# Kernel optimization log

Measured on AMD Instinct MI355X. Metric: run time of the kernel, lower is better.

The kernel has to match this reference:

```python
import jax, jax.numpy as jnp
import numpy as np
import math

B, S, E = 2, 2048, 2048
H, NOPE, ROPE, V, KVR, DOWN = 16, 64, 32, 64, 256, 2
QKD = NOPE + ROPE
SCALE = QKD ** -0.5
LOW = 4


def setup_inputs() -> dict:
    key = jax.random.key(0)
    ks = jax.random.split(key, 8)
    def w(k, shape):
        return jax.random.normal(k, shape, jnp.float32) * 0.02
    return {
        "hidden_states": jax.random.normal(ks[0], (B, S, E), jnp.float32),
        "wq": w(ks[1], (H * QKD, E)),
        "wkv_a": w(ks[2], (KVR + ROPE, E)),
        "kv_ln_g": jnp.ones((KVR,), jnp.float32),
        "kv_ln_b": jnp.zeros((KVR,), jnp.float32),
        "wkv_b": w(ks[3], (H * (NOPE + V), KVR)),
        "wo": w(ks[4], (E, H * V)),
        "fc_c_w": w(ks[5], (KVR // LOW, KVR)),
        "fc_c_b": jnp.zeros((KVR // LOW,), jnp.float32),
        "fc_p_w": w(ks[6], (KVR // LOW, KVR)),
        "fc_p_b": jnp.zeros((KVR // LOW,), jnp.float32),
    }


def _layernorm(x, g, b, eps=1e-5):
    m = jnp.mean(x, -1, keepdims=True)
    v = jnp.var(x, -1, keepdims=True)
    return (x - m) * jax.lax.rsqrt(v + eps) * g + b


def _pos_enc(T, d):
    # sinusoidal PE: even dims sin, odd dims cos (interleaved)
    pos = jnp.arange(T, dtype=jnp.float32)[:, None]
    div = jnp.exp(jnp.arange(0, d, 2, dtype=jnp.float32) * (-math.log(10000.0) / d))
    ang = pos * div[None, :]
    return jnp.stack([jnp.sin(ang), jnp.cos(ang)], -1).reshape(T, d)


def _rope(x, cos, sin):
    # complex multiply on adjacent pairs, matching torch.view_as_complex path
    xr = x.reshape(x.shape[:-1] + (-1, 2))
    x0, x1 = xr[..., 0], xr[..., 1]
    return jnp.stack([x0 * cos - x1 * sin, x0 * sin + x1 * cos], -1).reshape(x.shape)


def reference(hidden_states, wq, wkv_a, kv_ln_g, kv_ln_b, wkv_b, wo,
              fc_c_w, fc_c_b, fc_p_w, fc_p_b):
    # q projection -> split nope / rope parts
    q = (hidden_states @ wq.T).reshape(B, S, H, QKD)
    q_nope, q_pe = q[..., :NOPE], q[..., NOPE:]
    # low-rank kv projection -> latent + shared rope key
    kv = hidden_states @ wkv_a.T
    kv_c, k_pe = kv[..., :KVR], kv[..., KVR:]
    kv_c = _layernorm(kv_c, kv_ln_g, kv_ln_b)
    # inline partial RoPE (position_ids = arange)
    pos = jnp.arange(S, dtype=jnp.float32)
    freqs = 1.0 / (10000.0 ** (jnp.arange(0, ROPE, 2, dtype=jnp.float32) / ROPE))
    ang = pos[:, None] * freqs[None, :]  # (S, ROPE//2)
    cos, sin = jnp.cos(ang), jnp.sin(ang)
    q_pe = _rope(q_pe, cos[None, :, None, :], sin[None, :, None, :])
    k_pe = _rope(k_pe, cos[None, :, :], sin[None, :, :])
    # hypernetwork gate (train path): C from downsampled PE, repeat_interleave
    t = -(-S // DOWN)
    P = _pos_enc(S, KVR)
    C = jnp.repeat(_pos_enc(t, KVR), DOWN, axis=0)[:S]
    C2 = C @ fc_c_w.T + fc_c_b
    P2 = P @ fc_p_w.T + fc_p_b
    Wg = jax.nn.sigmoid(C2 @ P2.T)  # (S, S)
    r = jnp.arange(S)
    chunk = ((r[:, None] // DOWN) == (r[None, :] // DOWN)) & \
            ((r[:, None] % DOWN) >= (r[None, :] % DOWN))
    Wg = Wg * chunk.astype(Wg.dtype)
    # temporally merged latent KV (simulated compressed cache)
    kv_t = jnp.einsum('ts,bsc->btc', Wg, kv_c)
    k_pe_t = jnp.einsum('ts,bsr->btr', Wg, k_pe)
    # absorbed wkv_b: q_nope into latent space
    wkv_b3 = wkv_b.reshape(H, NOPE + V, KVR)
    q_abs = jnp.einsum('bshd,hdc->bshc', q_nope, wkv_b3[:, :NOPE])
    scores = (jnp.einsum('bshc,btc->bsht', q_abs, kv_t)
              + jnp.einsum('bshr,btr->bsht', q_pe, k_pe_t)) * SCALE
    # stride-aware causal mask: chunk-boundary keys + diagonal
    visible = ((r[None, :] <= r[:, None]) & (((r[None, :] + 1) % DOWN) == 0)) | \
              (r[None, :] == r[:, None])
    mask = jnp.where(visible, 0.0, -1e9).astype(scores.dtype)
    attn = jax.nn.softmax(scores + mask[:, None, :], axis=-1)
    x = jnp.einsum('bsht,btc->bshc', attn, kv_t)
    out = jnp.einsum('bshc,hdc->bshd', x, wkv_b3[:, NOPE:]).reshape(B, S, H * V)
    return out @ wo.T
```

## Files before the change

kernel.cpp:

```cpp
#include <hip/hip_runtime.h>
#include <hip/hip_bf16.h>
#include <math.h>
#include <stdint.h>

#define B_ 2
#define S_ 2048
#define E_ 2048
#define H_ 16
#define NOPE_ 64
#define ROPE_ 32
#define V_ 64
#define KVR_ 256
#define QKD_ 96
#define SCALE_ 0.10206207261596577f

typedef __hip_bfloat16 bf16;
typedef __attribute__((ext_vector_type(8))) short short8;
typedef __attribute__((ext_vector_type(4))) short short4v;
typedef __attribute__((ext_vector_type(4))) float floatx4;

__device__ __forceinline__ float bf2f(bf16 v) { return __bfloat162float(v); }
__device__ __forceinline__ float s2f(short v) {
    bf16 h = *reinterpret_cast<bf16*>(&v);
    return __bfloat162float(h);
}
__device__ __forceinline__ short f2bf_s(float f) {
    bf16 h = __float2bfloat16(f);
    return *reinterpret_cast<short*>(&h);
}
__device__ __forceinline__ void store_c(float* C, size_t i, float v) { C[i] = v; }
__device__ __forceinline__ void store_c(bf16* C, size_t i, float v) { C[i] = __float2bfloat16(v); }

__device__ __forceinline__ void g2l16(const bf16* g, bf16* l) {
    __builtin_amdgcn_global_load_lds(
        (const __attribute__((address_space(1))) void*)g,
        (__attribute__((address_space(3))) void*)l,
        16, 0, 0);
}

#define CV_N0 1048576
#define CV_N1 (CV_N0 + 393216)
#define CV_N2 (CV_N1 + 262144)
#define CV_N3 (CV_N2 + 65536)
#define CV_N4 (CV_N3 + 98304)
__global__ __launch_bounds__(256) void conv_fused_kernel(const float* __restrict__ hs,
                                                         const float* __restrict__ wq,
                                                         const float* __restrict__ wo,
                                                         const float* __restrict__ wkv_b,
                                                         const float* __restrict__ wkv_a,
                                                         bf16* __restrict__ hs_bf,
                                                         bf16* __restrict__ wq_bf,
                                                         bf16* __restrict__ wo_bf,
                                                         bf16* __restrict__ wkvb_bf,
                                                         bf16* __restrict__ wkva_pad) {
    int i = blockIdx.x * 256 + threadIdx.x;
    const float* src;
    bf16* dst;
    int j;
    if (i < CV_N0)      { src = hs;    dst = hs_bf;   j = i; }
    else if (i < CV_N1) { src = wq;    dst = wq_bf;   j = i - CV_N0; }
    else if (i < CV_N2) { src = wo;    dst = wo_bf;   j = i - CV_N1; }
    else if (i < CV_N3) { src = wkv_b; dst = wkvb_bf; j = i - CV_N2; }
    else if (i < CV_N4) {
        j = i - CV_N3;
        int row = j >> 8;
        short8 r;
        if (row < 288) {
            float4 a = ((const float4*)wkv_a)[2 * j];
            float4 b = ((const float4*)wkv_a)[2 * j + 1];
            r[0] = f2bf_s(a.x); r[1] = f2bf_s(a.y); r[2] = f2bf_s(a.z); r[3] = f2bf_s(a.w);
            r[4] = f2bf_s(b.x); r[5] = f2bf_s(b.y); r[6] = f2bf_s(b.z); r[7] = f2bf_s(b.w);
        } else {
            for (int k = 0; k < 8; ++k) r[k] = 0;
        }
        ((short8*)wkva_pad)[j] = r;
        return;
    } else return;
    float4 a = ((const float4*)src)[2 * j];
    float4 b = ((const float4*)src)[2 * j + 1];
    short8 r;
    r[0] = f2bf_s(a.x); r[1] = f2bf_s(a.y); r[2] = f2bf_s(a.z); r[3] = f2bf_s(a.w);
    r[4] = f2bf_s(b.x); r[5] = f2bf_s(b.y); r[6] = f2bf_s(b.z); r[7] = f2bf_s(b.w);
    ((short8*)dst)[j] = r;
}

__global__ __launch_bounds__(256) void transpose_wkvbT_kernel(const float* __restrict__ wkv_b,
                                                              bf16* __restrict__ wkvbT) {
    int h = blockIdx.x >> 3;
    int d0 = (blockIdx.x & 7) * 8;
    int c = threadIdx.x;
    short8 v;
#pragma unroll
    for (int j = 0; j < 8; ++j) v[j] = f2bf_s(wkv_b[(size_t)(h * 128 + d0 + j) * 256 + c]);
    *(short8*)(void*)&wkvbT[((size_t)h * 256 + c) * 64 + d0] = v;
}

template <typename TC>
__global__ __launch_bounds__(256, 3) void gemm_bt_lds(const bf16* __restrict__ A,
                                                      const bf16* __restrict__ Bm,
                                                      TC* __restrict__ C,
                                                      int M, int N, int K) {
    __shared__ bf16 Asf[128 * 32];
    __shared__ bf16 Bsf[128 * 32];
    int tid = threadIdx.x;
    int lane = tid & 63, w = tid >> 6;
    int q4 = lane >> 4, c16 = lane & 15;
    int wr = w >> 1, wc = w & 1;
    int m0 = blockIdx.y * 128, n0 = blockIdx.x * 128;
    floatx4 acc[4][4];
#pragma unroll
    for (int mi = 0; mi < 4; ++mi)
#pragma unroll
        for (int ni = 0; ni < 4; ++ni) acc[mi][ni] = (floatx4){0.f, 0.f, 0.f, 0.f};

    for (int k0 = 0; k0 < K; k0 += 32) {
        __syncthreads();
#pragma unroll
        for (int i = 0; i < 2; ++i) {
            int c = (w << 6) + lane + i * 256;
            int row = c >> 2, kc = c & 3;
            g2l16(&A[(size_t)(m0 + row) * K + k0 + kc * 8], &Asf[c * 8]);
            g2l16(&Bm[(size_t)(n0 + row) * K + k0 + kc * 8], &Bsf[c * 8]);
        }
        __syncthreads();
        short8 af[4], bfr[4];
#pragma unroll
        for (int mi = 0; mi < 4; ++mi)
            af[mi] = *(const short8*)(const void*)&Asf[(wr * 64 + mi * 16 + c16) * 32 + q4 * 8];
#pragma unroll
        for (int ni = 0; ni < 4; ++ni)
            bfr[ni] = *(const short8*)(const void*)&Bsf[(wc * 64 + ni * 16 + c16) * 32 + q4 * 8];
#pragma unroll
        for (int mi = 0; mi < 4; ++mi)
#pragma unroll
            for (int ni = 0; ni < 4; ++ni)
                acc[mi][ni] = __builtin_amdgcn_mfma_f32_16x16x32_bf16(af[mi], bfr[ni], acc[mi][ni], 0, 0, 0);
    }
#pragma unroll
    for (int mi = 0; mi < 4; ++mi)
#pragma unroll
        for (int ni = 0; ni < 4; ++ni)
#pragma unroll
            for (int r = 0; r < 4; ++r) {
                int row = m0 + wr * 64 + mi * 16 + q4 * 4 + r;
                int col = n0 + wc * 64 + ni * 16 + c16;
                store_c(C, (size_t)row * N + col, acc[mi][ni][r]);
            }
}

__global__ __launch_bounds__(256, 3) void gemm_qkv_fused(const bf16* __restrict__ A,
                                                         const bf16* __restrict__ Bq,
                                                         const bf16* __restrict__ Bkv,
                                                         bf16* __restrict__ Cq,
                                                         float* __restrict__ Ckv,
                                                         int K) {
    __shared__ bf16 Asf[128 * 32];
    __shared__ bf16 Bsf[128 * 32];
    int tid = threadIdx.x;
    int lane = tid & 63, w = tid >> 6;
    int q4 = lane >> 4, c16 = lane & 15;
    int wr = w >> 1, wc = w & 1;
    int bx = blockIdx.x;
    bool isq = bx < 12;
    const bf16* Bm = isq ? Bq : Bkv;
    int n0 = isq ? bx * 128 : (bx - 12) * 128;
    int m0 = blockIdx.y * 128;
    floatx4 acc[4][4];
#pragma unroll
    for (int mi = 0; mi < 4; ++mi)
#pragma unroll
        for (int ni = 0; ni < 4; ++ni) acc[mi][ni] = (floatx4){0.f, 0.f, 0.f, 0.f};

    for (int k0 = 0; k0 < K; k0 += 32) {
        __syncthreads();
#pragma unroll
        for (int i = 0; i < 2; ++i) {
            int c = (w << 6) + lane + i * 256;
            int row = c >> 2, kc = c & 3;
            g2l16(&A[(size_t)(m0 + row) * K + k0 + kc * 8], &Asf[c * 8]);
            g2l16(&Bm[(size_t)(n0 + row) * K + k0 + kc * 8], &Bsf[c * 8]);
        }
        __syncthreads();
        short8 af[4], bfr[4];
#pragma unroll
        for (int mi = 0; mi < 4; ++mi)
            af[mi] = *(const short8*)(const void*)&Asf[(wr * 64 + mi * 16 + c16) * 32 + q4 * 8];
#pragma unroll
        for (int ni = 0; ni < 4; ++ni)
            bfr[ni] = *(const short8*)(const void*)&Bsf[(wc * 64 + ni * 16 + c16) * 32 + q4 * 8];
#pragma unroll
        for (int mi = 0; mi < 4; ++mi)
#pragma unroll
            for (int ni = 0; ni < 4; ++ni)
                acc[mi][ni] = __builtin_amdgcn_mfma_f32_16x16x32_bf16(af[mi], bfr[ni], acc[mi][ni], 0, 0, 0);
    }
#pragma unroll
    for (int mi = 0; mi < 4; ++mi)
#pragma unroll
        for (int ni = 0; ni < 4; ++ni)
#pragma unroll
            for (int r = 0; r < 4; ++r) {
                int row = m0 + wr * 64 + mi * 16 + q4 * 4 + r;
                int col = n0 + wc * 64 + ni * 16 + c16;
                if (isq)
                    Cq[(size_t)row * 1536 + col] = __float2bfloat16(acc[mi][ni][r]);
                else
                    Ckv[(size_t)row * 384 + col] = acc[mi][ni][r];
            }
}

template <typename TC>
__global__ __launch_bounds__(256, 4) void gemm64_lds(const bf16* __restrict__ A, int lda, int aoffz,
                                                     const bf16* __restrict__ Bm, int ldb, int boffz,
                                                     TC* __restrict__ C, int ldc, int coffz,
                                                     int K, float scale) {
    int z = blockIdx.z;
    A += (size_t)z * aoffz;
    Bm += (size_t)z * boffz;
    C += (size_t)z * coffz;
    __shared__ bf16 Asf[64 * 32];
    __shared__ bf16 Bsf[64 * 32];
    int tid = threadIdx.x;
    int lane = tid & 63, w = tid >> 6;
    int q4 = lane >> 4, c16 = lane & 15;
    int m0 = blockIdx.y * 64, n0 = blockIdx.x * 64;
    floatx4 acc[4];
#pragma unroll
    for (int ni = 0; ni < 4; ++ni) acc[ni] = (floatx4){0.f, 0.f, 0.f, 0.f};
    int row = tid >> 2, kc = tid & 3;
    for (int k0 = 0; k0 < K; k0 += 32) {
        __syncthreads();
        g2l16(&A[(size_t)(m0 + row) * lda + k0 + kc * 8], &Asf[tid * 8]);
        g2l16(&Bm[(size_t)(n0 + row) * ldb + k0 + kc * 8], &Bsf[tid * 8]);
        __syncthreads();
        short8 af = *(const short8*)(const void*)&Asf[(w * 16 + c16) * 32 + q4 * 8];
#pragma unroll
        for (int ni = 0; ni < 4; ++ni) {
            short8 bfr = *(const short8*)(const void*)&Bsf[(ni * 16 + c16) * 32 + q4 * 8];
            acc[ni] = __builtin_amdgcn_mfma_f32_16x16x32_bf16(af, bfr, acc[ni], 0, 0, 0);
        }
    }
#pragma unroll
    for (int ni = 0; ni < 4; ++ni)
#pragma unroll
        for (int rr = 0; rr < 4; ++rr)
            store_c(C, (size_t)(m0 + w * 16 + q4 * 4 + rr) * ldc + n0 + ni * 16 + c16,
                    acc[ni][rr] * scale);
}

__global__ __launch_bounds__(256) void ln_rope_kernel(const float* __restrict__ kvraw,
                                                      const float* __restrict__ g,
                                                      const float* __restrict__ bta,
                                                      float* __restrict__ kv_c,
                                                      float* __restrict__ kpe) {
    int r = blockIdx.x;
    int tid = threadIdx.x;
    int lane = tid & 63, w = tid >> 6;
    float x = kvraw[(size_t)r * 384 + tid];
    float v1 = x, v2 = x * x;
#pragma unroll
    for (int o = 32; o; o >>= 1) { v1 += __shfl_down(v1, o); v2 += __shfl_down(v2, o); }
    __shared__ float s1[4], s2[4], stats[2];
    if (lane == 0) { s1[w] = v1; s2[w] = v2; }
    __syncthreads();
    if (tid == 0) {
        float S1 = s1[0] + s1[1] + s1[2] + s1[3];
        float S2 = s2[0] + s2[1] + s2[2] + s2[3];
        float mean = S1 / 256.0f;
        float var = S2 / 256.0f - mean * mean;
        stats[0] = mean;
        stats[1] = rsqrtf(var + 1e-5f);
    }
    __syncthreads();
    float y = (x - stats[0]) * stats[1] * g[tid] + bta[tid];
    kv_c[(size_t)r * 256 + tid] = y;
    if (tid < 16) {
        int j = tid;
        int s = r & (S_ - 1);
        float freq = expf(-(float)(2 * j) * 0.28782313662425572f);
        float ang = (float)s * freq;
        float c = cosf(ang), sn = sinf(ang);
        float x0 = kvraw[(size_t)r * 384 + 256 + 2 * j];
        float x1 = kvraw[(size_t)r * 384 + 256 + 2 * j + 1];
        kpe[(size_t)r * 32 + 2 * j]     = x0 * c - x1 * sn;
        kpe[(size_t)r * 32 + 2 * j + 1] = x0 * sn + x1 * c;
    }
}

__global__ __launch_bounds__(64) void c2p2_kernel(const float* __restrict__ fcw_c,
                                                  const float* __restrict__ fcb_c,
                                                  const float* __restrict__ fcw_p,
                                                  const float* __restrict__ fcb_p,
                                                  float* __restrict__ C2,
                                                  float* __restrict__ P2) {
    int t = blockIdx.x;
    int k = threadIdx.x;
    __shared__ float Crow[256], Prow[256];
    for (int i = k; i < 128; i += 64) {
        float div = expf(-(float)i * 0.07195578415606393f);
        float ap = (float)t * div;
        Prow[2 * i]     = sinf(ap);
        Prow[2 * i + 1] = cosf(ap);
        float ac = (float)(t >> 1) * div;
        Crow[2 * i]     = sinf(ac);
        Crow[2 * i + 1] = cosf(ac);
    }
    __syncthreads();
    float sc = fcb_c[k], sp = fcb_p[k];
    for (int c = 0; c < 256; ++c) {
        sc += Crow[c] * fcw_c[(size_t)k * 256 + c];
        sp += Prow[c] * fcw_p[(size_t)k * 256 + c];
    }
    C2[(size_t)t * 64 + k] = sc;
    P2[(size_t)t * 64 + k] = sp;
}

__global__ __launch_bounds__(256) void gates_kernel(const float* __restrict__ C2,
                                                    const float* __restrict__ P2,
                                                    float* __restrict__ g0,
                                                    float* __restrict__ g1) {
    int t = blockIdx.x * 256 + threadIdx.x;
    if (t >= S_) return;
    float d0 = 0.f;
    for (int k = 0; k < 64; ++k) d0 += C2[(size_t)t * 64 + k] * P2[(size_t)t * 64 + k];
    g0[t] = 1.0f / (1.0f + expf(-d0));
    float gg = 0.f;
    if (t & 1) {
        float d1 = 0.f;
        for (int k = 0; k < 64; ++k) d1 += C2[(size_t)t * 64 + k] * P2[(size_t)(t - 1) * 64 + k];
        gg = 1.0f / (1.0f + expf(-d1));
    }
    g1[t] = gg;
}

__global__ __launch_bounds__(256) void kve_kernel(const float* __restrict__ kv_c,
                                                  const float* __restrict__ kpe,
                                                  const float* __restrict__ g0,
                                                  const float* __restrict__ g1,
                                                  bf16* __restrict__ kve_full,
                                                  bf16* __restrict__ kvo) {
    int r = blockIdx.x, tid = threadIdx.x;
    int b = r >> 11, t = r & (S_ - 1);
    float a = g0[t], bb = g1[t];
    float v = a * kv_c[(size_t)r * 256 + tid];
    if (t & 1) v += bb * kv_c[(size_t)(r - 1) * 256 + tid];
    bf16 vb = __float2bfloat16(v);
    kve_full[(size_t)r * 288 + tid] = vb;
    if (t & 1) kvo[((size_t)b * 1024 + (t >> 1)) * 296 + tid] = vb;
    if (tid < 32) {
        float u = a * kpe[(size_t)r * 32 + tid];
        if (t & 1) u += bb * kpe[(size_t)(r - 1) * 32 + tid];
        bf16 ub = __float2bfloat16(u);
        kve_full[(size_t)r * 288 + 256 + tid] = ub;
        if (t & 1) kvo[((size_t)b * 1024 + (t >> 1)) * 296 + 256 + tid] = ub;
    }
}

__global__ __launch_bounds__(256) void kvoT32_kernel(const bf16* __restrict__ kvo,
                                                     bf16* __restrict__ kvoT) {
    int uch = blockIdx.x, b = blockIdx.y;
    int c = threadIdx.x;
    const bf16* src = kvo + ((size_t)b * 1024 + uch * 32) * 296 + c;
    short v[32];
#pragma unroll
    for (int j = 0; j < 32; ++j) v[j] = *(const short*)&src[(size_t)j * 296];
    bf16* dst = kvoT + (((size_t)b * 32 + uch) * 256 + c) * 32;
    int swz = (c >> 1) & 3;
#pragma unroll
    for (int q = 0; q < 4; ++q) {
        short8 o;
#pragma unroll
        for (int jj = 0; jj < 8; ++jj)
            o[jj] = (jj < 4) ? v[4 * q + jj] : v[16 + 4 * q + (jj - 4)];
        *(short8*)(void*)&dst[(q ^ swz) * 8] = o;
    }
}

__global__ __launch_bounds__(256) void rope_qe_kernel(const bf16* __restrict__ q,
                                                      bf16* __restrict__ qe) {
    int idx = blockIdx.x * 256 + threadIdx.x;
    if (idx >= B_ * S_ * H_ * 16) return;
    int j = idx & 15;
    int s = (idx >> 8) & (S_ - 1);
    float freq = expf(-(float)(2 * j) * 0.28782313662425572f);
    float ang = (float)s * freq;
    float c = cosf(ang), sn = sinf(ang);
    size_t row = idx >> 4;
    float a0 = bf2f(q[row * QKD_ + NOPE_ + 2 * j]);
    float a1 = bf2f(q[row * QKD_ + NOPE_ + 2 * j + 1]);
    qe[row * 288 + 256 + 2 * j]     = __float2bfloat16((a0 * c - a1 * sn) * SCALE_);
    qe[row * 288 + 256 + 2 * j + 1] = __float2bfloat16((a0 * sn + a1 * c) * SCALE_);
}

__global__ __launch_bounds__(256, 2) void attn8_kernel(const bf16* __restrict__ qe,
                                                       const bf16* __restrict__ kvo,
                                                       const bf16* __restrict__ kvoT,
                                                       const bf16* __restrict__ kve_full,
                                                       bf16* __restrict__ xout) {
    int s0 = (int)(gridDim.x - 1 - blockIdx.x) * 4;
    int b = blockIdx.y;
    int tid = threadIdx.x;
    int lane = tid & 63, w = tid >> 6;
    int q4 = lane >> 4, c16 = lane & 15;
    int s = s0 + w;
    int Nodd = (s + 1) >> 1;
    int NoddMax = (s0 + 4) >> 1;
    int niter = (NoddMax + 31) >> 5;

    __shared__ bf16 kvos[2][32][296];
    __shared__ bf16 kvts[2][256][32];
    __shared__ bf16 selfr[4][288];

    const bf16* kvob = kvo + (size_t)b * 1024 * 296;
    const bf16* kvoTb = kvoT + (size_t)b * 32 * 8192;

    if (tid < 144) {
        int rr = tid / 36, ch = tid - rr * 36;
        *(short8*)(void*)&selfr[rr][ch * 8] =
            *(const short8*)(const void*)&kve_full[(size_t)(b * S_ + s0 + rr) * 288 + ch * 8];
    }

    short8 qf[9];
    const bf16* qrow = qe + ((size_t)(b * S_ + s) * H_ + c16) * 288;
#pragma unroll
    for (int kk = 0; kk < 9; ++kk) qf[kk] = *(const short8*)(const void*)&qrow[kk * 32 + q4 * 8];

    floatx4 acc[16];
#pragma unroll
    for (int n = 0; n < 16; ++n) acc[n] = (floatx4){0.f, 0.f, 0.f, 0.f};
    float m_i = -1e30f, l_i = 0.f;
    int swz = (c16 >> 1) & 3;

    auto stage = [&](int t, int p) {
        const bf16* sa = kvob + (size_t)t * 32 * 296;
        bf16* la = &kvos[p][0][0];
#pragma unroll
        for (int i = 0; i < 4; ++i)
            g2l16(&sa[(size_t)(tid + i * 256) * 8], &la[(size_t)(tid + i * 256) * 8]);
        if (tid < 160) g2l16(&sa[(size_t)(tid + 1024) * 8], &la[(size_t)(tid + 1024) * 8]);
        const bf16* sb = kvoTb + (size_t)t * 8192;
        bf16* lb = &kvts[p][0][0];
#pragma unroll
        for (int i = 0; i < 4; ++i)
            g2l16(&sb[(size_t)(tid + i * 256) * 8], &lb[(size_t)(tid + i * 256) * 8]);
    };

    stage(0, 0);
    __syncthreads();

    float sdot = 0.f;
#pragma unroll
    for (int kk = 0; kk < 9; ++kk) {
        short8 kv8 = *(const short8*)(const void*)&selfr[w][kk * 32 + q4 * 8];
#pragma unroll
        for (int j = 0; j < 8; ++j) sdot += s2f(qf[kk][j]) * s2f(kv8[j]);
    }
    sdot += __shfl_xor(sdot, 16);
    sdot += __shfl_xor(sdot, 32);

    for (int it = 0; it < niter; ++it) {
        int p = it & 1;
        if (it + 1 < niter) stage(it + 1, 1 - p);

        int u0 = it * 32;
        floatx4 ca0 = (floatx4){0.f, 0.f, 0.f, 0.f}, ca1 = (floatx4){0.f, 0.f, 0.f, 0.f};
        floatx4 cb0 = (floatx4){0.f, 0.f, 0.f, 0.f}, cb1 = (floatx4){0.f, 0.f, 0.f, 0.f};
        __builtin_amdgcn_s_setprio(1);
#pragma unroll
        for (int kk = 0; kk < 9; ++kk) {
            short8 avA = *(const short8*)(const void*)&kvos[p][c16][kk * 32 + q4 * 8];
            short8 avB = *(const short8*)(const void*)&kvos[p][16 + c16][kk * 32 + q4 * 8];
            if (kk & 1) {
                ca1 = __builtin_amdgcn_mfma_f32_16x16x32_bf16(avA, qf[kk], ca1, 0, 0, 0);
                cb1 = __builtin_amdgcn_mfma_f32_16x16x32_bf16(avB, qf[kk], cb1, 0, 0, 0);
            } else {
                ca0 = __builtin_amdgcn_mfma_f32_16x16x32_bf16(avA, qf[kk], ca0, 0, 0, 0);
                cb0 = __builtin_amdgcn_mfma_f32_16x16x32_bf16(avB, qf[kk], cb0, 0, 0, 0);
            }
        }
        __builtin_amdgcn_s_setprio(0);
        floatx4 cA = ca0 + ca1;
        floatx4 cB = cb0 + cb1;
        int kA = u0 + q4 * 4;
        int kB = u0 + 16 + q4 * 4;
#pragma unroll
        for (int r = 0; r < 4; ++r) {
            if (kA + r >= Nodd) cA[r] = -1e30f;
            if (kB + r >= Nodd) cB[r] = -1e30f;
        }
        float tmax = fmaxf(fmaxf(fmaxf(cA[0], cA[1]), fmaxf(cA[2], cA[3])),
                           fmaxf(fmaxf(cB[0], cB[1]), fmaxf(cB[2], cB[3])));
        tmax = fmaxf(tmax, __shfl_xor(tmax, 16));
        tmax = fmaxf(tmax, __shfl_xor(tmax, 32));
        float mn = fmaxf(m_i, tmax);
        bool chg = mn > m_i;
        float al = __expf(m_i - mn);
        float pA0 = __expf(cA[0] - mn), pA1 = __expf(cA[1] - mn);
        float pA2 = __expf(cA[2] - mn), pA3 = __expf(cA[3] - mn);
        float pB0 = __expf(cB[0] - mn), pB1 = __expf(cB[1] - mn);
        float pB2 = __expf(cB[2] - mn), pB3 = __expf(cB[3] - mn);
        float rs = (pA0 + pA1 + pA2 + pA3) + (pB0 + pB1 + pB2 + pB3);
        rs += __shfl_xor(rs, 16);
        rs += __shfl_xor(rs, 32);
        l_i = l_i * al + rs;
        m_i = mn;
        if (__any(chg)) {
#pragma unroll
            for (int n = 0; n < 16; ++n) {
                acc[n][0] *= al; acc[n][1] *= al; acc[n][2] *= al; acc[n][3] *= al;
            }
        }
        short8 pf;
        pf[0] = f2bf_s(pA0); pf[1] = f2bf_s(pA1); pf[2] = f2bf_s(pA2); pf[3] = f2bf_s(pA3);
        pf[4] = f2bf_s(pB0); pf[5] = f2bf_s(pB1); pf[6] = f2bf_s(pB2); pf[7] = f2bf_s(pB3);
        __builtin_amdgcn_s_setprio(1);
#pragma unroll
        for (int n = 0; n < 16; ++n) {
            short8 a8 = *(const short8*)(const void*)&kvts[p][n * 16 + c16][(q4 ^ swz) * 8];
            acc[n] = __builtin_amdgcn_mfma_f32_16x16x32_bf16(a8, pf, acc[n], 0, 0, 0);
        }
        __builtin_amdgcn_s_setprio(0);
        __syncthreads();
    }

    if ((s & 1) == 0) {
        float mn = fmaxf(m_i, sdot);
        float al = __expf(m_i - mn);
        float pp = __expf(sdot - mn);
        l_i = l_i * al + pp;
        m_i = mn;
#pragma unroll
        for (int n = 0; n < 16; ++n) {
            short4v kv4 = *(const short4v*)(const void*)&selfr[w][n * 16 + q4 * 4];
#pragma unroll
            for (int r = 0; r < 4; ++r)
                acc[n][r] = acc[n][r] * al + pp * s2f(kv4[r]);
        }
    }

    float invl = 1.0f / l_i;
    bf16* orow = xout + ((size_t)(b * S_ + s) * H_ + c16) * 256;
#pragma unroll
    for (int n = 0; n < 16; ++n) {
        short4v o;
        o[0] = f2bf_s(acc[n][0] * invl);
        o[1] = f2bf_s(acc[n][1] * invl);
        o[2] = f2bf_s(acc[n][2] * invl);
        o[3] = f2bf_s(acc[n][3] * invl);
        *(short4v*)(void*)&orow[n * 16 + q4 * 4] = o;
    }
}

extern "C" void kernel_launch(void* const* d_in, const int* in_sizes, int n_in,
                              void* d_out, int out_size, void* d_ws, size_t ws_size,
                              hipStream_t stream) {
    const float* hs     = (const float*)d_in[0];
    const float* wq     = (const float*)d_in[1];
    const float* wkv_a  = (const float*)d_in[2];
    const float* ln_g   = (const float*)d_in[3];
    const float* ln_b   = (const float*)d_in[4];
    const float* wkv_b  = (const float*)d_in[5];
    const float* wo     = (const float*)d_in[6];
    const float* fc_c_w = (const float*)d_in[7];
    const float* fc_c_b = (const float*)d_in[8];
    const float* fc_p_w = (const float*)d_in[9];
    const float* fc_p_b = (const float*)d_in[10];
    float* out = (float*)d_out;
    (void)in_sizes; (void)n_in; (void)out_size; (void)ws_size;

    const int M = B_ * S_;
    char* wsb = (char*)d_ws;
    size_t o = 0;
    auto alloc = [&](size_t bytes) { char* p = wsb + o; o += (bytes + 255) & ~(size_t)255; return p; };

    bf16* qe = (bf16*)alloc((size_t)M * H_ * 288 * 2);
    char* region2 = alloc((size_t)M * H_ * 256 * 2);
    bf16* hs_bf    = (bf16*)region2;
    bf16* wq_bf    = (bf16*)(region2 + (size_t)M * E_ * 2);
    bf16* wkva_pad = (bf16*)(region2 + (size_t)M * E_ * 2 + (size_t)1536 * E_ * 2);
    bf16* x_bf     = (bf16*)region2;
    char* region3 = alloc((size_t)M * 1536 * 2);
    bf16* q_bf    = (bf16*)region3;
    bf16* outp_bf = (bf16*)region3;
    float* kvraw = (float*)alloc((size_t)M * 384 * 4);
    float* kv_c  = (float*)alloc((size_t)M * 256 * 4);
    float* kpe   = (float*)alloc((size_t)M * 32 * 4);
    bf16* wo_bf   = (bf16*)alloc((size_t)E_ * 1024 * 2);
    bf16* wkvb_bf = (bf16*)alloc((size_t)2048 * 256 * 2);
    bf16* wkvbT   = (bf16*)alloc((size_t)H_ * 256 * 64 * 2);
    bf16* kve_full = (bf16*)alloc((size_t)M * 288 * 2);
    bf16* kvo      = (bf16*)alloc((size_t)B_ * 1024 * 296 * 2);
    bf16* kvoT     = (bf16*)alloc((size_t)B_ * 32 * 8192 * 2);
    float* C2 = (float*)alloc((size_t)S_ * 64 * 4);
    float* P2 = (float*)alloc((size_t)S_ * 64 * 4);
    float* g0 = (float*)alloc(S_ * 4);
    float* g1 = (float*)alloc(S_ * 4);

    conv_fused_kernel<<<(CV_N4 + 255) / 256, 256, 0, stream>>>(
        hs, wq, wo, wkv_b, wkv_a, hs_bf, wq_bf, wo_bf, wkvb_bf, wkva_pad);
    transpose_wkvbT_kernel<<<H_ * 8, 256, 0, stream>>>(wkv_b, wkvbT);
    gemm_qkv_fused<<<dim3(15, M / 128), 256, 0, stream>>>(hs_bf, wq_bf, wkva_pad, q_bf, kvraw, E_);
    ln_rope_kernel<<<M, 256, 0, stream>>>(kvraw, ln_g, ln_b, kv_c, kpe);
    c2p2_kernel<<<S_, 64, 0, stream>>>(fc_c_w, fc_c_b, fc_p_w, fc_p_b, C2, P2);
    gates_kernel<<<(S_ + 255) / 256, 256, 0, stream>>>(C2, P2, g0, g1);
    kve_kernel<<<M, 256, 0, stream>>>(kv_c, kpe, g0, g1, kve_full, kvo);
    kvoT32_kernel<<<dim3(32, B_), 256, 0, stream>>>(kvo, kvoT);
    gemm64_lds<bf16><<<dim3(256 / 64, M / 64, H_), 256, 0, stream>>>(
        q_bf, H_ * QKD_, QKD_, wkvbT, 64, 256 * 64, qe, H_ * 288, 288, 64, SCALE_);
    rope_qe_kernel<<<(M * H_ * 16 + 255) / 256, 256, 0, stream>>>(q_bf, qe);
    attn8_kernel<<<dim3(S_ / 4, B_), 256, 0, stream>>>(qe, kvo, kvoT, kve_full, x_bf);
    gemm64_lds<bf16><<<dim3(1, M / 64, H_), 256, 0, stream>>>(
        x_bf, H_ * 256, 256, wkvb_bf + (size_t)64 * 256, 256, 128 * 256, outp_bf, 1024, 64, 256, 1.0f);
    gemm_bt_lds<float><<<dim3(E_ / 128, M / 128), 256, 0, stream>>>(outp_bf, wo_bf, out, M, E_, 1024);
}
```

Baseline: 349.9 us.

## Fuse preprocessing kernels, retile QKV GEMM to 64-row tiles with XCD remap

Folds the wkv_b transpose into the conversion kernel, and merges layernorm, RoPE and gated KV merging into one kernel that handles row pairs. The C2/P2 projection and gate kernels become a single kernel using a wave reduction. The QKV GEMM moves to 64x128 tiles over a 1D grid of 960 blocks, with a block-index remap that spreads tiles across XCDs. The output GEMM launch bound drops from 3 to 2 blocks per CU. Together these cut kernel launches and intermediate fp32 round trips, at the risk of lower per-block MFMA reuse in the QKV GEMM.

Result: faster. 338.5 us (-3.3%).

```diff
diff --git a/kernel.cpp b/kernel.cpp
--- a/kernel.cpp
+++ b/kernel.cpp
@@ -43,6 +43,7 @@
 #define CV_N2 (CV_N1 + 262144)
 #define CV_N3 (CV_N2 + 65536)
 #define CV_N4 (CV_N3 + 98304)
+#define CV_N5 (CV_N4 + 32768)
 __global__ __launch_bounds__(256) void conv_fused_kernel(const float* __restrict__ hs,
                                                          const float* __restrict__ wq,
                                                          const float* __restrict__ wo,
@@ -52,7 +53,8 @@
                                                          bf16* __restrict__ wq_bf,
                                                          bf16* __restrict__ wo_bf,
                                                          bf16* __restrict__ wkvb_bf,
-                                                         bf16* __restrict__ wkva_pad) {
+                                                         bf16* __restrict__ wkva_pad,
+                                                         bf16* __restrict__ wkvbT) {
     int i = blockIdx.x * 256 + threadIdx.x;
     const float* src;
     bf16* dst;
@@ -75,6 +77,18 @@
         }
         ((short8*)wkva_pad)[j] = r;
         return;
+    } else if (i < CV_N5) {
+        j = i - CV_N4;
+        int h = j >> 11;
+        int rem = j & 2047;
+        int d0 = (rem >> 8) * 8;
+        int c = rem & 255;
+        short8 v;
+#pragma unroll
+        for (int jj = 0; jj < 8; ++jj)
+            v[jj] = f2bf_s(wkv_b[(size_t)(h * 128 + d0 + jj) * 256 + c]);
+        *(short8*)(void*)&wkvbT[((size_t)h * 256 + c) * 64 + d0] = v;
+        return;
     } else return;
     float4 a = ((const float4*)src)[2 * j];
     float4 b = ((const float4*)src)[2 * j + 1];
@@ -84,19 +98,8 @@
     ((short8*)dst)[j] = r;
 }
 
-__global__ __launch_bounds__(256) void transpose_wkvbT_kernel(const float* __restrict__ wkv_b,
-                                                              bf16* __restrict__ wkvbT) {
-    int h = blockIdx.x >> 3;
-    int d0 = (blockIdx.x & 7) * 8;
-    int c = threadIdx.x;
-    short8 v;
-#pragma unroll
-    for (int j = 0; j < 8; ++j) v[j] = f2bf_s(wkv_b[(size_t)(h * 128 + d0 + j) * 256 + c]);
-    *(short8*)(void*)&wkvbT[((size_t)h * 256 + c) * 64 + d0] = v;
-}
-
 template <typename TC>
-__global__ __launch_bounds__(256, 3) void gemm_bt_lds(const bf16* __restrict__ A,
+__global__ __launch_bounds__(256, 2) void gemm_bt_lds(const bf16* __restrict__ A,
                                                       const bf16* __restrict__ Bm,
                                                       TC* __restrict__ C,
                                                       int M, int N, int K) {
@@ -148,59 +151,65 @@
             }
 }
 
-__global__ __launch_bounds__(256, 3) void gemm_qkv_fused(const bf16* __restrict__ A,
-                                                         const bf16* __restrict__ Bq,
-                                                         const bf16* __restrict__ Bkv,
-                                                         bf16* __restrict__ Cq,
-                                                         float* __restrict__ Ckv,
-                                                         int K) {
-    __shared__ bf16 Asf[128 * 32];
+__global__ __launch_bounds__(256) void gemm_qkv_fused64(const bf16* __restrict__ A,
+                                                        const bf16* __restrict__ Bq,
+                                                        const bf16* __restrict__ Bkv,
+                                                        bf16* __restrict__ Cq,
+                                                        float* __restrict__ Ckv,
+                                                        int K) {
+    int bid = blockIdx.x;
+    int orig = (bid & 7) * 120 + (bid >> 3);
+    int by = orig / 15, bx = orig % 15;
+    bool isq = bx < 12;
+    const bf16* Bm = isq ? Bq : Bkv;
+    int n0 = isq ? bx * 128 : (bx - 12) * 128;
+    int m0 = by * 64;
+    __shared__ bf16 Asf[64 * 32];
     __shared__ bf16 Bsf[128 * 32];
     int tid = threadIdx.x;
     int lane = tid & 63, w = tid >> 6;
     int q4 = lane >> 4, c16 = lane & 15;
     int wr = w >> 1, wc = w & 1;
-    int bx = blockIdx.x;
-    bool isq = bx < 12;
-    const bf16* Bm = isq ? Bq : Bkv;
-    int n0 = isq ? bx * 128 : (bx - 12) * 128;
-    int m0 = blockIdx.y * 128;
-    floatx4 acc[4][4];
-#pragma unroll
-    for (int mi = 0; mi < 4; ++mi)
+    floatx4 acc[2][4];
+#pragma unroll
+    for (int mi = 0; mi < 2; ++mi)
 #pragma unroll
         for (int ni = 0; ni < 4; ++ni) acc[mi][ni] = (floatx4){0.f, 0.f, 0.f, 0.f};
 
     for (int k0 = 0; k0 < K; k0 += 32) {
         __syncthreads();
-#pragma unroll
-        for (int i = 0; i < 2; ++i) {
-            int c = (w << 6) + lane + i * 256;
+        {
+            int c = tid;
             int row = c >> 2, kc = c & 3;
             g2l16(&A[(size_t)(m0 + row) * K + k0 + kc * 8], &Asf[c * 8]);
+        }
+#pragma unroll
+        for (int i = 0; i < 2; ++i) {
+            int c = tid + i * 256;
+            int row = c >> 2, kc = c & 3;
             g2l16(&Bm[(size_t)(n0 + row) * K + k0 + kc * 8], &Bsf[c * 8]);
         }
         __syncthreads();
-        short8 af[4], bfr[4];
-#pragma unroll
-        for (int mi = 0; mi < 4; ++mi)
-            af[mi] = *(const short8*)(const void*)&Asf[(wr * 64 + mi * 16 + c16) * 32 + q4 * 8];
+        short8 af[2], bfr[4];
+#pragma unroll
+        for (int mi = 0; mi < 2; ++mi)
+            af[mi] = *(const short8*)(const void*)&Asf[(wr * 32 + mi * 16 + c16) * 32 + q4 * 8];
 #pragma unroll
         for (int ni = 0; ni < 4; ++ni)
             bfr[ni] = *(const short8*)(const void*)&Bsf[(wc * 64 + ni * 16 + c16) * 32 + q4 * 8];
 #pragma unroll
-        for (int mi = 0; mi < 4; ++mi)
+        for (int mi = 0; mi < 2; ++mi)
 #pragma unroll
             for (int ni = 0; ni < 4; ++ni)
                 acc[mi][ni] = __builtin_amdgcn_mfma_f32_16x16x32_bf16(af[mi], bfr[ni], acc[mi][ni], 0, 0, 0);
     }
 #pragma unroll
-    for (int mi = 0; mi < 4; ++mi)
+    for (int mi = 0; mi < 2; ++mi)
 #pragma unroll
         for (int ni = 0; ni < 4; ++ni)
 #pragma unroll
             for (int r = 0; r < 4; ++r) {
-                int row = m0 + wr * 64 + mi * 16 + q4 * 4 + r;
+                int row = m0 + wr * 32 + mi * 16 + q4 * 4 + r;
                 int col = n0 + wc * 64 + ni * 16 + c16;
                 if (isq)
                     Cq[(size_t)row * 1536 + col] = __float2bfloat16(acc[mi][ni][r]);
@@ -248,54 +257,15 @@
                     acc[ni][rr] * scale);
 }
 
-__global__ __launch_bounds__(256) void ln_rope_kernel(const float* __restrict__ kvraw,
-                                                      const float* __restrict__ g,
-                                                      const float* __restrict__ bta,
-                                                      float* __restrict__ kv_c,
-                                                      float* __restrict__ kpe) {
-    int r = blockIdx.x;
-    int tid = threadIdx.x;
-    int lane = tid & 63, w = tid >> 6;
-    float x = kvraw[(size_t)r * 384 + tid];
-    float v1 = x, v2 = x * x;
-#pragma unroll
-    for (int o = 32; o; o >>= 1) { v1 += __shfl_down(v1, o); v2 += __shfl_down(v2, o); }
-    __shared__ float s1[4], s2[4], stats[2];
-    if (lane == 0) { s1[w] = v1; s2[w] = v2; }
-    __syncthreads();
-    if (tid == 0) {
-        float S1 = s1[0] + s1[1] + s1[2] + s1[3];
-        float S2 = s2[0] + s2[1] + s2[2] + s2[3];
-        float mean = S1 / 256.0f;
-        float var = S2 / 256.0f - mean * mean;
-        stats[0] = mean;
-        stats[1] = rsqrtf(var + 1e-5f);
-    }
-    __syncthreads();
-    float y = (x - stats[0]) * stats[1] * g[tid] + bta[tid];
-    kv_c[(size_t)r * 256 + tid] = y;
-    if (tid < 16) {
-        int j = tid;
-        int s = r & (S_ - 1);
-        float freq = expf(-(float)(2 * j) * 0.28782313662425572f);
-        float ang = (float)s * freq;
-        float c = cosf(ang), sn = sinf(ang);
-        float x0 = kvraw[(size_t)r * 384 + 256 + 2 * j];
-        float x1 = kvraw[(size_t)r * 384 + 256 + 2 * j + 1];
-        kpe[(size_t)r * 32 + 2 * j]     = x0 * c - x1 * sn;
-        kpe[(size_t)r * 32 + 2 * j + 1] = x0 * sn + x1 * c;
-    }
-}
-
-__global__ __launch_bounds__(64) void c2p2_kernel(const float* __restrict__ fcw_c,
-                                                  const float* __restrict__ fcb_c,
-                                                  const float* __restrict__ fcw_p,
-                                                  const float* __restrict__ fcb_p,
-                                                  float* __restrict__ C2,
-                                                  float* __restrict__ P2) {
+__global__ __launch_bounds__(64) void c2p2g_kernel(const float* __restrict__ fcw_c,
+                                                   const float* __restrict__ fcb_c,
+                                                   const float* __restrict__ fcw_p,
+                                                   const float* __restrict__ fcb_p,
+                                                   float* __restrict__ g0,
+                                                   float* __restrict__ g1) {
     int t = blockIdx.x;
     int k = threadIdx.x;
-    __shared__ float Crow[256], Prow[256];
+    __shared__ float Crow[256], Prow[256], Pprev[256];
     for (int i = k; i < 128; i += 64) {
         float div = expf(-(float)i * 0.07195578415606393f);
         float ap = (float)t * div;
@@ -304,55 +274,93 @@
         float ac = (float)(t >> 1) * div;
         Crow[2 * i]     = sinf(ac);
         Crow[2 * i + 1] = cosf(ac);
+        float app = (float)(t - 1) * div;
+        Pprev[2 * i]     = sinf(app);
+        Pprev[2 * i + 1] = cosf(app);
     }
     __syncthreads();
-    float sc = fcb_c[k], sp = fcb_p[k];
+    float sc = fcb_c[k], sp = fcb_p[k], spp = fcb_p[k];
     for (int c = 0; c < 256; ++c) {
-        sc += Crow[c] * fcw_c[(size_t)k * 256 + c];
-        sp += Prow[c] * fcw_p[(size_t)k * 256 + c];
-    }
-    C2[(size_t)t * 64 + k] = sc;
-    P2[(size_t)t * 64 + k] = sp;
-}
-
-__global__ __launch_bounds__(256) void gates_kernel(const float* __restrict__ C2,
-                                                    const float* __restrict__ P2,
-                                                    float* __restrict__ g0,
-                                                    float* __restrict__ g1) {
-    int t = blockIdx.x * 256 + threadIdx.x;
-    if (t >= S_) return;
-    float d0 = 0.f;
-    for (int k = 0; k < 64; ++k) d0 += C2[(size_t)t * 64 + k] * P2[(size_t)t * 64 + k];
-    g0[t] = 1.0f / (1.0f + expf(-d0));
-    float gg = 0.f;
-    if (t & 1) {
-        float d1 = 0.f;
-        for (int k = 0; k < 64; ++k) d1 += C2[(size_t)t * 64 + k] * P2[(size_t)(t - 1) * 64 + k];
-        gg = 1.0f / (1.0f + expf(-d1));
-    }
-    g1[t] = gg;
-}
-
-__global__ __launch_bounds__(256) void kve_kernel(const float* __restrict__ kv_c,
-                                                  const float* __restrict__ kpe,
-                                                  const float* __restrict__ g0,
-                                                  const float* __restrict__ g1,
-                                                  bf16* __restrict__ kve_full,
-                                                  bf16* __restrict__ kvo) {
-    int r = blockIdx.x, tid = threadIdx.x;
-    int b = r >> 11, t = r & (S_ - 1);
-    float a = g0[t], bb = g1[t];
-    float v = a * kv_c[(size_t)r * 256 + tid];
-    if (t & 1) v += bb * kv_c[(size_t)(r - 1) * 256 + tid];
-    bf16 vb = __float2bfloat16(v);
-    kve_full[(size_t)r * 288 + tid] = vb;
-    if (t & 1) kvo[((size_t)b * 1024 + (t >> 1)) * 296 + tid] = vb;
-    if (tid < 32) {
-        float u = a * kpe[(size_t)r * 32 + tid];
-        if (t & 1) u += bb * kpe[(size_t)(r - 1) * 32 + tid];
-        bf16 ub = __float2bfloat16(u);
-        kve_full[(size_t)r * 288 + 256 + tid] = ub;
-        if (t & 1) kvo[((size_t)b * 1024 + (t >> 1)) * 296 + 256 + tid] = ub;
+        float wc_ = fcw_c[(size_t)k * 256 + c];
+        float wp_ = fcw_p[(size_t)k * 256 + c];
+        sc += Crow[c] * wc_;
+        sp += Prow[c] * wp_;
+        spp += Pprev[c] * wp_;
+    }
+    float d0 = sc * sp, d1 = sc * spp;
+#pragma unroll
+    for (int o = 32; o; o >>= 1) {
+        d0 += __shfl_down(d0, o);
+        d1 += __shfl_down(d1, o);
+    }
+    if (k == 0) {
+        g0[t] = 1.0f / (1.0f + expf(-d0));
+        g1[t] = (t & 1) ? 1.0f / (1.0f + expf(-d1)) : 0.f;
+    }
+}
+
+__global__ __launch_bounds__(256) void lnkve_kernel(const float* __restrict__ kvraw,
+                                                    const float* __restrict__ g,
+                                                    const float* __restrict__ bta,
+                                                    const float* __restrict__ g0,
+                                                    const float* __restrict__ g1,
+                                                    bf16* __restrict__ kve_full,
+                                                    bf16* __restrict__ kvo) {
+    int pb = blockIdx.x;
+    int b = pb >> 10, u = pb & 1023;
+    int t0 = 2 * u, t1 = 2 * u + 1;
+    size_t r0 = (size_t)b * S_ + t0, r1 = r0 + 1;
+    int tid = threadIdx.x;
+    int lane = tid & 63, w = tid >> 6;
+    float x0 = kvraw[r0 * 384 + tid];
+    float x1 = kvraw[r1 * 384 + tid];
+    float s0 = x0, q0 = x0 * x0, s1 = x1, q1 = x1 * x1;
+#pragma unroll
+    for (int o = 32; o; o >>= 1) {
+        s0 += __shfl_down(s0, o); q0 += __shfl_down(q0, o);
+        s1 += __shfl_down(s1, o); q1 += __shfl_down(q1, o);
+    }
+    __shared__ float red[4][4];
+    __shared__ float st[4];
+    if (lane == 0) { red[w][0] = s0; red[w][1] = q0; red[w][2] = s1; red[w][3] = q1; }
+    __syncthreads();
+    if (tid == 0) {
+        float S0 = red[0][0] + red[1][0] + red[2][0] + red[3][0];
+        float Q0 = red[0][1] + red[1][1] + red[2][1] + red[3][1];
+        float S1 = red[0][2] + red[1][2] + red[2][2] + red[3][2];
+        float Q1 = red[0][3] + red[1][3] + red[2][3] + red[3][3];
+        float m0 = S0 / 256.0f, m1 = S1 / 256.0f;
+        st[0] = m0; st[1] = rsqrtf(Q0 / 256.0f - m0 * m0 + 1e-5f);
+        st[2] = m1; st[3] = rsqrtf(Q1 / 256.0f - m1 * m1 + 1e-5f);
+    }
+    __syncthreads();
+    float gg = g[tid], bb_ = bta[tid];
+    float y0 = (x0 - st[0]) * st[1] * gg + bb_;
+    float y1 = (x1 - st[2]) * st[3] * gg + bb_;
+    float a0 = g0[t0], a1 = g0[t1], b1 = g1[t1];
+    kve_full[r0 * 288 + tid] = __float2bfloat16(a0 * y0);
+    float vo = a1 * y1 + b1 * y0;
+    bf16 vob = __float2bfloat16(vo);
+    kve_full[r1 * 288 + tid] = vob;
+    kvo[((size_t)b * 1024 + u) * 296 + tid] = vob;
+    if (tid < 16) {
+        int j = tid;
+        float freq = expf(-(float)(2 * j) * 0.28782313662425572f);
+        float a00 = (float)t0 * freq, a01 = (float)t1 * freq;
+        float c0 = cosf(a00), sn0 = sinf(a00);
+        float c1 = cosf(a01), sn1 = sinf(a01);
+        float e00 = kvraw[r0 * 384 + 256 + 2 * j], e01 = kvraw[r0 * 384 + 256 + 2 * j + 1];
+        float e10 = kvraw[r1 * 384 + 256 + 2 * j], e11 = kvraw[r1 * 384 + 256 + 2 * j + 1];
+        float k00 = e00 * c0 - e01 * sn0, k01 = e00 * sn0 + e01 * c0;
+        float k10 = e10 * c1 - e11 * sn1, k11 = e10 * sn1 + e11 * c1;
+        kve_full[r0 * 288 + 256 + 2 * j]     = __float2bfloat16(a0 * k00);
+        kve_full[r0 * 288 + 256 + 2 * j + 1] = __float2bfloat16(a0 * k01);
+        float u0 = a1 * k10 + b1 * k00, u1 = a1 * k11 + b1 * k01;
+        bf16 u0b = __float2bfloat16(u0), u1b = __float2bfloat16(u1);
+        kve_full[r1 * 288 + 256 + 2 * j]     = u0b;
+        kve_full[r1 * 288 + 256 + 2 * j + 1] = u1b;
+        kvo[((size_t)b * 1024 + u) * 296 + 256 + 2 * j]     = u0b;
+        kvo[((size_t)b * 1024 + u) * 296 + 256 + 2 * j + 1] = u1b;
     }
 }
 
@@ -583,27 +591,20 @@
     bf16* q_bf    = (bf16*)region3;
     bf16* outp_bf = (bf16*)region3;
     float* kvraw = (float*)alloc((size_t)M * 384 * 4);
-    float* kv_c  = (float*)alloc((size_t)M * 256 * 4);
-    float* kpe   = (float*)alloc((size_t)M * 32 * 4);
     bf16* wo_bf   = (bf16*)alloc((size_t)E_ * 1024 * 2);
     bf16* wkvb_bf = (bf16*)alloc((size_t)2048 * 256 * 2);
     bf16* wkvbT   = (bf16*)alloc((size_t)H_ * 256 * 64 * 2);
     bf16* kve_full = (bf16*)alloc((size_t)M * 288 * 2);
     bf16* kvo      = (bf16*)alloc((size_t)B_ * 1024 * 296 * 2);
     bf16* kvoT     = (bf16*)alloc((size_t)B_ * 32 * 8192 * 2);
-    float* C2 = (float*)alloc((size_t)S_ * 64 * 4);
-    float* P2 = (float*)alloc((size_t)S_ * 64 * 4);
     float* g0 = (float*)alloc(S_ * 4);
     float* g1 = (float*)alloc(S_ * 4);
 
-    conv_fused_kernel<<<(CV_N4 + 255) / 256, 256, 0, stream>>>(
-        hs, wq, wo, wkv_b, wkv_a, hs_bf, wq_bf, wo_bf, wkvb_bf, wkva_pad);
-    transpose_wkvbT_kernel<<<H_ * 8, 256, 0, stream>>>(wkv_b, wkvbT);
-    gemm_qkv_fused<<<dim3(15, M / 128), 256, 0, stream>>>(hs_bf, wq_bf, wkva_pad, q_bf, kvraw, E_);
-    ln_rope_kernel<<<M, 256, 0, stream>>>(kvraw, ln_g, ln_b, kv_c, kpe);
-    c2p2_kernel<<<S_, 64, 0, stream>>>(fc_c_w, fc_c_b, fc_p_w, fc_p_b, C2, P2);
-    gates_kernel<<<(S_ + 255) / 256, 256, 0, stream>>>(C2, P2, g0, g1);
-    kve_kernel<<<M, 256, 0, stream>>>(kv_c, kpe, g0, g1, kve_full, kvo);
+    conv_fused_kernel<<<(CV_N5 + 255) / 256, 256, 0, stream>>>(
+        hs, wq, wo, wkv_b, wkv_a, hs_bf, wq_bf, wo_bf, wkvb_bf, wkva_pad, wkvbT);
+    gemm_qkv_fused64<<<960, 256, 0, stream>>>(hs_bf, wq_bf, wkva_pad, q_bf, kvraw, E_);
+    c2p2g_kernel<<<S_, 64, 0, stream>>>(fc_c_w, fc_c_b, fc_p_w, fc_p_b, g0, g1);
+    lnkve_kernel<<<B_ * 1024, 256, 0, stream>>>(kvraw, ln_g, ln_b, g0, g1, kve_full, kvo);
     kvoT32_kernel<<<dim3(32, B_), 256, 0, stream>>>(kvo, kvoT);
     gemm64_lds<bf16><<<dim3(256 / 64, M / 64, H_), 256, 0, stream>>>(
         q_bf, H_ * QKD_, QKD_, wkvbT, 64, 256 * 64, qe, H_ * 288, 288, 64, SCALE_);
```
